# Kernel optimization log

Measured on AMD Instinct MI355X. Metric: run time of the kernel, lower is better.

Reference implementation:

```python
import jax, jax.numpy as jnp
import numpy as np

EMBED_DIM = 1024
PROJ_DIM = 64
B, S = 8, 2048


def setup_inputs() -> dict:
    key = jax.random.key(0)
    k1, k2, k3 = jax.random.split(key, 3)
    context = jax.random.normal(k1, (S, B, EMBED_DIM), dtype=jnp.float32)
    prior = jax.random.uniform(k2, (B, S), dtype=jnp.float32)
    # xavier_uniform for (2*proj_dim, embed_dim)
    bound = float(np.sqrt(6.0 / (2 * PROJ_DIM + EMBED_DIM)))
    proj_weight = jax.random.uniform(k3, (2 * PROJ_DIM, EMBED_DIM), dtype=jnp.float32,
                                     minval=-bound, maxval=bound)
    proj_bias = jnp.zeros((2 * PROJ_DIM,), dtype=jnp.float32)
    return {"context": context, "prior": prior,
            "proj_weight": proj_weight, "proj_bias": proj_bias}


def reference(context, prior, proj_weight, proj_bias):
    # context: (S, B, E) -> (B, S, E)
    x = jnp.transpose(context, (1, 0, 2))
    b, s, e = x.shape
    qk = jnp.einsum('bse,pe->bsp', x, proj_weight) + proj_bias  # (B,S,2P)
    query, key = jnp.split(qk, 2, axis=2)
    # neighbor scores, scaled by embed_dim (as in the original)
    fwd = jnp.sum(query[:, :-1] * key[:, 1:], axis=-1) / e   # (B,S-1) score i<->i+1
    bwd = jnp.sum(query[:, 1:] * key[:, :-1], axis=-1) / e   # (B,S-1) score i<->i-1
    ninf = jnp.full((b, 1), -jnp.inf, dtype=x.dtype)
    score = jnp.stack([jnp.concatenate([fwd, ninf], axis=1),
                       jnp.concatenate([ninf, bwd], axis=1)], axis=-1)  # (B,S,2)
    prob = jax.nn.softmax(score, axis=-1)
    # torch .roll(shifts=-1) with no dims flattens the whole tensor: reproduce that
    shift_prob = jnp.roll(prob[:, :, 1].reshape(-1), -1).reshape(b, s)
    prob0 = jnp.sqrt(prob[:, :, 0] * shift_prob + 1e-6)      # (B,S)
    neighbor_attn = prior + (1.0 - prior) * prob0
    log_prob = jnp.log(neighbor_attn)
    # Original places log_prob[:, :-1] on the superdiagonal and hits it with
    # triu matmuls on both sides: C[i,j] = sum_{m=i}^{j-1} log_prob[m] for j>i.
    # Equivalent O(n^2): prefix sums cs[t] = sum_{m<t} log_prob[m].
    cs = jnp.concatenate([jnp.zeros((b, 1), dtype=x.dtype),
                          jnp.cumsum(log_prob[:, :-1], axis=1)], axis=1)  # (B,S)
    D = cs[:, None, :] - cs[:, :, None]            # D[b,i,j] = cs[j]-cs[i]
    i_idx = jnp.arange(s)
    upper = i_idx[None, :] > i_idx[:, None]        # (S,S) j>i
    M = jnp.where(upper[None], D, -D)              # C + C^T (symmetric)
    constituent_attn = jnp.exp(M)
    diag = i_idx[None, :] == i_idx[:, None]
    constituent_attn = jnp.where(diag[None], jnp.zeros((), x.dtype), constituent_attn)
    return constituent_attn, neighbor_attn
```

## Files before the change

### kernel.cpp

```cpp
#include <hip/hip_runtime.h>
#include <hip/hip_bf16.h>
#include <cstdint>
#include <cstddef>

#define E_DIM 1024
#define PD 64
#define NP 128
#define B_DIM 8
#define S_DIM 2048
#define M_TOT (B_DIM * S_DIM)

#define BMR 32
#define BK 32
#define NCH (E_DIM / BK)

typedef __attribute__((ext_vector_type(8))) short short8v;
typedef __attribute__((ext_vector_type(4))) float f32x4;

__device__ __forceinline__ void gload16(const void* g, void* l) {
    __builtin_amdgcn_global_load_lds(
        (const __attribute__((address_space(1))) unsigned int*)g,
        (__attribute__((address_space(3))) unsigned int*)(uintptr_t)l,
        16, 0, 0);
}

__device__ __forceinline__ unsigned pk_rn(float a, float b) {
    float2 p; p.x = a; p.y = b;
    __hip_bfloat162 h2 = __float22bfloat162_rn(p);
    unsigned r;
    __builtin_memcpy(&r, &h2, sizeof(r));
    return r;
}

__device__ __forceinline__ void cvt_hilo(const f32x4 v0, const f32x4 v1,
                                         short8v& h, short8v& l) {
    union { unsigned u[4]; short8v s; } H, L;
    H.u[0] = pk_rn(v0.x, v0.y);
    H.u[1] = pk_rn(v0.z, v0.w);
    H.u[2] = pk_rn(v1.x, v1.y);
    H.u[3] = pk_rn(v1.z, v1.w);
    const float r0 = v0.x - __uint_as_float(H.u[0] << 16);
    const float r1 = v0.y - __uint_as_float(H.u[0] & 0xFFFF0000u);
    const float r2 = v0.z - __uint_as_float(H.u[1] << 16);
    const float r3 = v0.w - __uint_as_float(H.u[1] & 0xFFFF0000u);
    const float r4 = v1.x - __uint_as_float(H.u[2] << 16);
    const float r5 = v1.y - __uint_as_float(H.u[2] & 0xFFFF0000u);
    const float r6 = v1.z - __uint_as_float(H.u[3] << 16);
    const float r7 = v1.w - __uint_as_float(H.u[3] & 0xFFFF0000u);
    L.u[0] = pk_rn(r0, r1);
    L.u[1] = pk_rn(r2, r3);
    L.u[2] = pk_rn(r4, r5);
    L.u[3] = pk_rn(r6, r7);
    h = H.s; l = L.s;
}

__global__ __launch_bounds__(256) void conv_w(const float* __restrict__ W,
                                              ushort* __restrict__ hiImg,
                                              ushort* __restrict__ loImg) {
    const int t = blockIdx.x * 256 + threadIdx.x;
    const int c  = t & 127;
    const int q  = (t >> 7) & 3;
    const int ch = t >> 9;
    const float* src = W + (size_t)c * E_DIM + ch * 32 + q * 8;
    const f32x4 v0 = *(const f32x4*)src;
    const f32x4 v1 = *(const f32x4*)(src + 4);
    short8v h, l;
    cvt_hilo(v0, v1, h, l);
    const size_t off = ((size_t)(ch * 4 + q) * NP + c) * 8;
    *(short8v*)&hiImg[off] = h;
    *(short8v*)&loImg[off] = l;
}

__global__ __launch_bounds__(256, 2) void gemm_qk(const float* __restrict__ A,
                                                  const ushort* __restrict__ hiImg,
                                                  const ushort* __restrict__ loImg,
                                                  const float* __restrict__ bias,
                                                  float* __restrict__ qk) {
    __shared__ __align__(16) float  As[3][BMR][BK];
    __shared__ __align__(16) ushort Whi[3][4][NP][8];
    __shared__ __align__(16) ushort Wlo[3][4][NP][8];
    const int tid = threadIdx.x;
    const int m0  = blockIdx.x * BMR;
    const int w   = __builtin_amdgcn_readfirstlane(tid >> 6);
    const int ln  = tid & 63;
    const int lr  = ln >> 3;
    const int g8  = ln & 7;
    const int row16 = ln & 15;
    const int kq    = ln >> 4;
    const int r7    = row16 & 7;
    const int sg0 = ((((kq << 1) | 0) ^ r7) & 7) << 2;
    const int sg1 = ((((kq << 1) | 1) ^ r7) & 7) << 2;

    const float*  aS = A + (size_t)(m0 + w * 8 + lr) * E_DIM + ((g8 ^ lr) << 2);
    const ushort* hS = hiImg + (size_t)(w * 2) * 512 + ln * 8;
    const ushort* lS = loImg + (size_t)(w * 2) * 512 + ln * 8;

    float bias2[2];
    bias2[0] = bias[w * 32 + row16];
    bias2[1] = bias[w * 32 + 16 + row16];

    f32x4 acc[2][2];
#pragma unroll
    for (int i = 0; i < 2; ++i)
#pragma unroll
        for (int j = 0; j < 2; ++j) acc[i][j] = (f32x4){0.f, 0.f, 0.f, 0.f};

#define STAGE(BUF, CH)                                                          \
    {                                                                           \
        gload16(aS + (size_t)(CH) * BK, &As[BUF][w * 8][0]);                    \
        gload16(hS + (size_t)(CH) * 4096,       (ushort*)Whi[BUF] + (w * 2) * 512);       \
        gload16(hS + (size_t)(CH) * 4096 + 512, (ushort*)Whi[BUF] + (w * 2 + 1) * 512);   \
        gload16(lS + (size_t)(CH) * 4096,       (ushort*)Wlo[BUF] + (w * 2) * 512);       \
        gload16(lS + (size_t)(CH) * 4096 + 512, (ushort*)Wlo[BUF] + (w * 2 + 1) * 512);   \
    }

    STAGE(0, 0)
    STAGE(1, 1)

#pragma unroll
    for (int ch = 0; ch < NCH; ++ch) {
        const int buf = ch % 3;
        if (ch == NCH - 1) {
            asm volatile("s_waitcnt vmcnt(0)" ::: "memory");
        } else {
            asm volatile("s_waitcnt vmcnt(5)" ::: "memory");
        }
        __builtin_amdgcn_sched_barrier(0);
        __builtin_amdgcn_s_barrier();
        if (ch + 2 < NCH) {
            STAGE((ch + 2) % 3, ch + 2)
        }
        short8v ah[2], al[2];
#pragma unroll
        for (int fi = 0; fi < 2; ++fi) {
            const float* base = &As[buf][fi * 16 + row16][0];
            const f32x4 v0 = *(const f32x4*)(base + sg0);
            const f32x4 v1 = *(const f32x4*)(base + sg1);
            cvt_hilo(v0, v1, ah[fi], al[fi]);
        }
        short8v wh[2], wl[2];
#pragma unroll
        for (int fj = 0; fj < 2; ++fj) {
            wh[fj] = *(const short8v*)&Whi[buf][kq][w * 32 + fj * 16 + row16][0];
            wl[fj] = *(const short8v*)&Wlo[buf][kq][w * 32 + fj * 16 + row16][0];
        }
#pragma unroll
        for (int fi = 0; fi < 2; ++fi)
#pragma unroll
            for (int fj = 0; fj < 2; ++fj) {
                acc[fi][fj] = __builtin_amdgcn_mfma_f32_16x16x32_bf16(
                    ah[fi], wh[fj], acc[fi][fj], 0, 0, 0);
                acc[fi][fj] = __builtin_amdgcn_mfma_f32_16x16x32_bf16(
                    ah[fi], wl[fj], acc[fi][fj], 0, 0, 0);
                acc[fi][fj] = __builtin_amdgcn_mfma_f32_16x16x32_bf16(
                    al[fi], wh[fj], acc[fi][fj], 0, 0, 0);
            }
    }
#undef STAGE

#pragma unroll
    for (int fi = 0; fi < 2; ++fi)
#pragma unroll
        for (int fj = 0; fj < 2; ++fj) {
#pragma unroll
            for (int r = 0; r < 4; ++r) {
                const int m = m0 + fi * 16 + kq * 4 + r;
                const int p = w * 32 + fj * 16 + row16;
                qk[(size_t)m * NP + p] = acc[fi][fj][r] + bias2[fj];
            }
        }
}

__global__ __launch_bounds__(256) void neighbor_probs(const float* __restrict__ qk,
                                                      float* __restrict__ p0,
                                                      float* __restrict__ p1) {
    const int m = blockIdx.x * 4 + (threadIdx.x >> 6);
    const int lane = threadIdx.x & 63;
    const int s = m >> 3;
    const int b = m & 7;

    const float q = qk[(size_t)m * NP + lane];
    const float kn = (s < S_DIM - 1) ? qk[(size_t)(m + B_DIM) * NP + PD + lane] : 0.f;
    const float kp = (s > 0) ? qk[(size_t)(m - B_DIM) * NP + PD + lane] : 0.f;
    float f = q * kn;
    float g = q * kp;
#pragma unroll
    for (int off = 32; off; off >>= 1) {
        f += __shfl_xor(f, off);
        g += __shfl_xor(g, off);
    }
    if (lane == 0) {
        const float s0 = f * (1.f / (float)E_DIM);
        const float s1 = g * (1.f / (float)E_DIM);
        float P0, P1;
        if (s == S_DIM - 1) { P0 = 0.f; P1 = 1.f; }
        else if (s == 0)    { P0 = 1.f; P1 = 0.f; }
        else {
            const float mx = fmaxf(s0, s1);
            const float e0 = __expf(s0 - mx), e1 = __expf(s1 - mx);
            const float inv = 1.f / (e0 + e1);
            P0 = e0 * inv; P1 = e1 * inv;
        }
        p0[b * S_DIM + s] = P0;
        p1[b * S_DIM + s] = P1;
    }
}

__global__ __launch_bounds__(256) void combine_scan(const float* __restrict__ p0,
                                                    const float* __restrict__ p1,
                                                    const float* __restrict__ prior,
                                                    float* __restrict__ out_na,
                                                    float* __restrict__ cs) {
    const int b = blockIdx.x;
    const int tid = threadIdx.x;
    __shared__ float sh[256];

    const int base = b * S_DIM + tid * 8;
    float incl[8];
    float run = 0.f;
#pragma unroll
    for (int u = 0; u < 8; ++u) {
        const int fidx = base + u;
        int nf = fidx + 1;
        if (nf == B_DIM * S_DIM) nf = 0;
        const float P0 = p0[fidx];
        const float sp = p1[nf];
        const float pr = prior[fidx];
        const float na = pr + (1.f - pr) * sqrtf(P0 * sp + 1e-6f);
        out_na[fidx] = na;
        run += __logf(na);
        incl[u] = run;
    }
    sh[tid] = run;
    __syncthreads();
    for (int off = 1; off < 256; off <<= 1) {
        float v = sh[tid];
        if (tid >= off) v += sh[tid - off];
        __syncthreads();
        sh[tid] = v;
        __syncthreads();
    }
    const float offset = (tid > 0) ? sh[tid - 1] : 0.f;
#pragma unroll
    for (int u = 0; u < 8; ++u) {
        cs[base + u] = offset + ((u > 0) ? incl[u - 1] : 0.f);
    }
}

__global__ __launch_bounds__(256) void big_out(const float* __restrict__ cs,
                                               float* __restrict__ out) {
    const int bi = blockIdx.x;
    const int b = bi >> 11;
    const int i = bi & (S_DIM - 1);
    const float ci = cs[b * S_DIM + i];
    const float* crow = cs + (size_t)b * S_DIM;
    float* orow = out + (size_t)bi * S_DIM;
    const int j0 = threadIdx.x * 8;
#pragma unroll
    for (int h = 0; h < 2; ++h) {
        const int j = j0 + h * 4;
        const f32x4 cj = *(const f32x4*)&crow[j];
        f32x4 o;
        {
            const int jj = j + 0; const float m = (jj > i) ? (cj.x - ci) : (ci - cj.x);
            o.x = (jj == i) ? 0.f : __expf(m);
        }
        {
            const int jj = j + 1; const float m = (jj > i) ? (cj.y - ci) : (ci - cj.y);
            o.y = (jj == i) ? 0.f : __expf(m);
        }
        {
            const int jj = j + 2; const float m = (jj > i) ? (cj.z - ci) : (ci - cj.z);
            o.z = (jj == i) ? 0.f : __expf(m);
        }
        {
            const int jj = j + 3; const float m = (jj > i) ? (cj.w - ci) : (ci - cj.w);
            o.w = (jj == i) ? 0.f : __expf(m);
        }
        *(f32x4*)&orow[j] = o;
    }
}

extern "C" void kernel_launch(void* const* d_in, const int* in_sizes, int n_in,
                              void* d_out, int out_size, void* d_ws, size_t ws_size,
                              hipStream_t stream) {
    const float* context = (const float*)d_in[0];
    const float* prior   = (const float*)d_in[1];
    const float* W       = (const float*)d_in[2];
    const float* bias    = (const float*)d_in[3];
    float* out = (float*)d_out;

    float* qk = (float*)d_ws;
    float* p0 = qk + (size_t)M_TOT * NP;
    float* p1 = p0 + M_TOT;
    float* cs = p1 + M_TOT;
    ushort* hiImg = (ushort*)out;
    ushort* loImg = hiImg + (size_t)NP * E_DIM;
    float* na_out = out + (size_t)B_DIM * S_DIM * S_DIM;

    conv_w<<<64, 256, 0, stream>>>(W, hiImg, loImg);
    gemm_qk<<<M_TOT / BMR, 256, 0, stream>>>(context, hiImg, loImg, bias, qk);
    neighbor_probs<<<M_TOT / 4, 256, 0, stream>>>(qk, p0, p1);
    combine_scan<<<B_DIM, 256, 0, stream>>>(p0, p1, prior, na_out, cs);
    big_out<<<M_TOT, 256, 0, stream>>>(cs, out);
}
```

Baseline: 64.75 us.

## Fuse neighbor score computation into per-batch scan kernel

Merges the neighbor dot-product/softmax kernel and the combine/prefix-scan kernel into one kernel with one 1024-thread block per batch. Each thread computes two positions' forward and backward scores with vectorized loads. The P1 shift is done through shared memory instead of global p0/p1 buffers. This drops a launch and the intermediate global round trip. The cost is that the whole qk read now runs on only 8 blocks, each with strided, poorly coalesced row loads, which limits memory parallelism.

Result: slower. 110.2 us (+70.2%).

```diff
diff --git a/kernel.cpp b/kernel.cpp
--- a/kernel.cpp
+++ b/kernel.cpp
@@ -171,80 +171,71 @@
         }
 }
 
-__global__ __launch_bounds__(256) void neighbor_probs(const float* __restrict__ qk,
-                                                      float* __restrict__ p0,
-                                                      float* __restrict__ p1) {
-    const int m = blockIdx.x * 4 + (threadIdx.x >> 6);
-    const int lane = threadIdx.x & 63;
-    const int s = m >> 3;
-    const int b = m & 7;
-
-    const float q = qk[(size_t)m * NP + lane];
-    const float kn = (s < S_DIM - 1) ? qk[(size_t)(m + B_DIM) * NP + PD + lane] : 0.f;
-    const float kp = (s > 0) ? qk[(size_t)(m - B_DIM) * NP + PD + lane] : 0.f;
-    float f = q * kn;
-    float g = q * kp;
-#pragma unroll
-    for (int off = 32; off; off >>= 1) {
-        f += __shfl_xor(f, off);
-        g += __shfl_xor(g, off);
-    }
-    if (lane == 0) {
-        const float s0 = f * (1.f / (float)E_DIM);
-        const float s1 = g * (1.f / (float)E_DIM);
+__global__ __launch_bounds__(1024) void scores_scan(const float* __restrict__ qk,
+                                                    const float* __restrict__ prior,
+                                                    float* __restrict__ out_na,
+                                                    float* __restrict__ cs) {
+    __shared__ float shP1[S_DIM];
+    __shared__ float shScan[1024];
+    const int b = blockIdx.x;
+    const int tid = threadIdx.x;
+
+    float P0v[2], P1v[2];
+#pragma unroll
+    for (int u = 0; u < 2; ++u) {
+        const int s = tid * 2 + u;
         float P0, P1;
-        if (s == S_DIM - 1) { P0 = 0.f; P1 = 1.f; }
-        else if (s == 0)    { P0 = 1.f; P1 = 0.f; }
+        if (s == 0)              { P0 = 1.f; P1 = 0.f; }
+        else if (s == S_DIM - 1) { P0 = 0.f; P1 = 1.f; }
         else {
+            const int m = s * B_DIM + b;
+            const f32x4* qv = (const f32x4*)(qk + (size_t)m * NP);
+            const f32x4* kf = (const f32x4*)(qk + (size_t)(m + B_DIM) * NP + PD);
+            const f32x4* kb = (const f32x4*)(qk + (size_t)(m - B_DIM) * NP + PD);
+            float f = 0.f, g = 0.f;
+#pragma unroll
+            for (int i = 0; i < 16; ++i) {
+                const f32x4 q4 = qv[i];
+                const f32x4 f4 = kf[i];
+                const f32x4 b4 = kb[i];
+                f += q4.x * f4.x + q4.y * f4.y + q4.z * f4.z + q4.w * f4.w;
+                g += q4.x * b4.x + q4.y * b4.y + q4.z * b4.z + q4.w * b4.w;
+            }
+            const float s0 = f * (1.f / (float)E_DIM);
+            const float s1 = g * (1.f / (float)E_DIM);
             const float mx = fmaxf(s0, s1);
             const float e0 = __expf(s0 - mx), e1 = __expf(s1 - mx);
             const float inv = 1.f / (e0 + e1);
             P0 = e0 * inv; P1 = e1 * inv;
         }
-        p0[b * S_DIM + s] = P0;
-        p1[b * S_DIM + s] = P1;
-    }
-}
-
-__global__ __launch_bounds__(256) void combine_scan(const float* __restrict__ p0,
-                                                    const float* __restrict__ p1,
-                                                    const float* __restrict__ prior,
-                                                    float* __restrict__ out_na,
-                                                    float* __restrict__ cs) {
-    const int b = blockIdx.x;
-    const int tid = threadIdx.x;
-    __shared__ float sh[256];
-
-    const int base = b * S_DIM + tid * 8;
-    float incl[8];
-    float run = 0.f;
-#pragma unroll
-    for (int u = 0; u < 8; ++u) {
-        const int fidx = base + u;
-        int nf = fidx + 1;
-        if (nf == B_DIM * S_DIM) nf = 0;
-        const float P0 = p0[fidx];
-        const float sp = p1[nf];
-        const float pr = prior[fidx];
-        const float na = pr + (1.f - pr) * sqrtf(P0 * sp + 1e-6f);
-        out_na[fidx] = na;
-        run += __logf(na);
-        incl[u] = run;
-    }
-    sh[tid] = run;
+        P0v[u] = P0; P1v[u] = P1;
+        shP1[s] = P1;
+    }
     __syncthreads();
-    for (int off = 1; off < 256; off <<= 1) {
-        float v = sh[tid];
-        if (tid >= off) v += sh[tid - off];
+
+    float lg[2];
+#pragma unroll
+    for (int u = 0; u < 2; ++u) {
+        const int s = tid * 2 + u;
+        const float sp = (s == S_DIM - 1) ? 0.f : shP1[s + 1];
+        const float pr = prior[b * S_DIM + s];
+        const float na = pr + (1.f - pr) * sqrtf(P0v[u] * sp + 1e-6f);
+        out_na[b * S_DIM + s] = na;
+        lg[u] = __logf(na);
+    }
+    const float run = lg[0] + lg[1];
+    shScan[tid] = run;
+    __syncthreads();
+    for (int off = 1; off < 1024; off <<= 1) {
+        float v = shScan[tid];
+        if (tid >= off) v += shScan[tid - off];
         __syncthreads();
-        sh[tid] = v;
+        shScan[tid] = v;
         __syncthreads();
     }
-    const float offset = (tid > 0) ? sh[tid - 1] : 0.f;
-#pragma unroll
-    for (int u = 0; u < 8; ++u) {
-        cs[base + u] = offset + ((u > 0) ? incl[u - 1] : 0.f);
-    }
+    const float offset = (tid > 0) ? shScan[tid - 1] : 0.f;
+    cs[b * S_DIM + tid * 2]     = offset;
+    cs[b * S_DIM + tid * 2 + 1] = offset + lg[0];
 }
 
 __global__ __launch_bounds__(256) void big_out(const float* __restrict__ cs,
@@ -291,16 +282,13 @@
     float* out = (float*)d_out;
 
     float* qk = (float*)d_ws;
-    float* p0 = qk + (size_t)M_TOT * NP;
-    float* p1 = p0 + M_TOT;
-    float* cs = p1 + M_TOT;
+    float* cs = qk + (size_t)M_TOT * NP;
     ushort* hiImg = (ushort*)out;
     ushort* loImg = hiImg + (size_t)NP * E_DIM;
     float* na_out = out + (size_t)B_DIM * S_DIM * S_DIM;
 
     conv_w<<<64, 256, 0, stream>>>(W, hiImg, loImg);
     gemm_qk<<<M_TOT / BMR, 256, 0, stream>>>(context, hiImg, loImg, bias, qk);
-    neighbor_probs<<<M_TOT / 4, 256, 0, stream>>>(qk, p0, p1);
-    combine_scan<<<B_DIM, 256, 0, stream>>>(p0, p1, prior, na_out, cs);
+    scores_scan<<<B_DIM, 1024, 0, stream>>>(qk, prior, na_out, cs);
     big_out<<<M_TOT, 256, 0, stream>>>(cs, out);
 }
```
